# Kernel optimization log

Hardware: AMD Instinct MI355X
Metric: run time of the kernel (lower is better)

## Reference

```python
import jax, jax.numpy as jnp
import numpy as np

B, S, D, C = 16, 1024, 768, 2


def setup_inputs() -> dict:
    key = jax.random.key(0)
    ks = jax.random.split(key, 6)
    sc = 1.0 / np.sqrt(D)
    return {
        "tokens": jax.random.normal(ks[0], (B, S, D), jnp.float32),
        "Wk": jax.random.normal(ks[1], (D, D), jnp.float32) * sc,
        "bk": jnp.zeros((D,), jnp.float32),
        "Wq": jax.random.normal(ks[2], (D, D), jnp.float32) * sc,
        "bq": jnp.zeros((D,), jnp.float32),
        "Wv": jax.random.normal(ks[3], (D, D), jnp.float32) * sc,
        "bv": jnp.zeros((D,), jnp.float32),
        "ln_g": jnp.ones((S, D), jnp.float32),
        "ln_b": jnp.zeros((S, D), jnp.float32),
        "W_sgsa": jax.random.normal(ks[4], (D, 1), jnp.float32) * sc,
        "b_sgsa": jnp.zeros((1,), jnp.float32),
        "W_fnn": jax.random.normal(ks[5], (4 * D, C), jnp.float32) * (1.0 / np.sqrt(4 * D)),
        "b_fnn": jnp.zeros((C,), jnp.float32),
    }


def reference(tokens, Wk, bk, Wq, bq, Wv, bv, ln_g, ln_b, W_sgsa, b_sgsa, W_fnn, b_fnn):
    fact = 1.0 / jnp.sqrt(jnp.asarray(D, tokens.dtype))
    # --- token-wise single-head attention ---
    K = tokens @ Wk + bk                                  # [B,S,D]
    Q = tokens @ Wq + bq
    V = tokens @ Wv + bv
    att = jax.nn.softmax(jnp.einsum('bsd,btd->bst', Q, K) * fact, axis=-1)  # [B,S,S]
    out = jnp.einsum('bst,btd->bsd', att, V)              # [B,S,D]
    # --- LayerNorm over last two dims (S,D) jointly, eps=1e-8 ---
    mu = jnp.mean(out, axis=(1, 2), keepdims=True)
    var = jnp.var(out, axis=(1, 2), keepdims=True)
    out_ln = (out - mu) / jnp.sqrt(var + 1e-8) * ln_g + ln_b
    # --- feature-wise attention (same K/Q/V weights, transposed bmm) ---
    K_N = out_ln @ Wk + bk
    Q_N = out_ln @ Wq + bq
    V_N = out_ln @ Wv + bv
    att_N = jax.nn.softmax(jnp.einsum('bsd,bse->bde', Q_N, K_N) * fact, axis=-1)  # [B,D,D]
    out_N = jnp.einsum('bsd,bde->bse', V_N, att_N)        # [B,S,D]
    # --- SGSA gating ---
    gate = out_N @ W_sgsa + b_sgsa                        # [B,S,1]
    out_sgsa = gate * out_N                               # [B,S,D]
    # --- concat, dual pooling, FC ---
    cat = jnp.concatenate([tokens, out_sgsa], axis=2)     # [B,S,2D]
    pooled = jnp.concatenate([jnp.mean(cat, axis=1), jnp.max(cat, axis=1)], axis=1)  # [B,4D]
    return pooled @ W_fnn + b_fnn                         # [B,C]
```

## Files before the change

### kernel.cpp

```cpp
#include <hip/hip_runtime.h>

#define BB 16
#define SS 1024
#define DD 768

typedef _Float16 f16x4 __attribute__((ext_vector_type(4)));
typedef _Float16 f16x8 __attribute__((ext_vector_type(8)));
typedef float f32x4 __attribute__((ext_vector_type(4)));

__device__ __forceinline__ void gload_lds16(const void* g, void* l) {
  __builtin_amdgcn_global_load_lds(
      (const __attribute__((address_space(1))) unsigned int*)g,
      (__attribute__((address_space(3))) unsigned int*)l, 16, 0, 0);
}

template<int OUTM, int BIAS>
__global__ __launch_bounds__(512) void gemm256(
    const _Float16* __restrict__ A, long long aB,
    const _Float16* __restrict__ Bt, long long bB,
    const float* __restrict__ bias, int biasB,
    void* __restrict__ Cv, long long cB,
    int M, int N, int K)
{
  __shared__ __attribute__((aligned(16))) _Float16 lds[65536];
  const int t = threadIdx.x;
  int z, m0, n0;
  if (OUTM == 3 || OUTM == 4) {
    z = blockIdx.x / 3;
    n0 = (blockIdx.x % 3) * 256;
    m0 = blockIdx.y * 256;
  } else {
    z = blockIdx.z;
    m0 = blockIdx.x * 256;
    n0 = blockIdx.y * 256;
  }
  const _Float16* Ab = A + (size_t)z * aB;
  const _Float16* Bb = Bt + (size_t)z * bB;

  const int l = t & 63, w = t >> 6;
  const int wr = (w >> 2) * 128, wc = (w & 3) * 64;
  const int lrow = l & 15, kq = l >> 4;
  const int p2 = lrow >> 1;
  const int qread = ((lrow & 1) << 2) | (kq ^ (p2 & 3));
  const int fragoff = p2 * 128 + qread * 16;

  const int sp = t >> 3, sq = t & 7;
  const int srow = 2 * sp + (sq >> 2);
  const int schk = (sq & 3) ^ (sp & 3);
  const size_t ldK = (size_t)K * 2;
  const char* pA0 = (const char*)Ab + (size_t)(m0 + srow) * ldK + schk * 16;
  const char* pA1 = pA0 + (size_t)128 * ldK;
  const char* pB0 = (const char*)Bb + (size_t)(n0 + srow) * ldK + schk * 16;
  const char* pB1 = pB0 + (size_t)128 * ldK;
  char* const ldsb = (char*)lds;
  const int dstt = t * 16;

  auto stg = [&](int mat, int s, int T, int sd) {
    const char* g0 = (mat ? pB0 : pA0) + (size_t)T * 128 + s * 64;
    const char* g1 = (mat ? pB1 : pA1) + (size_t)T * 128 + s * 64;
    char* d = ldsb + sd * 65536 + mat * 32768 + s * 16384 + dstt;
    gload_lds16(g0, d);
    gload_lds16(g1, d + 8192);
  };

  f32x4 acc[8][4] = {};
  f16x8 af[4], bfr[4];

#define LOAD_B(S) { _Pragma("unroll") for (int n = 0; n < 4; n++) \
    bfr[n] = *(const f16x8*)(Bbase + (S) * 16384 + (wc + n * 16) * 64 + fragoff); }
#define LOAD_A(S, QM) { _Pragma("unroll") for (int mi = 0; mi < 4; mi++) \
    af[mi] = *(const f16x8*)(Abase + (S) * 16384 + (wr + (QM) * 64 + mi * 16) * 64 + fragoff); }
#define MFMA16(QM) { __builtin_amdgcn_s_setprio(1); \
    _Pragma("unroll") for (int mi = 0; mi < 4; mi++) { \
      _Pragma("unroll") for (int n = 0; n < 4; n++) \
        acc[(QM) * 4 + mi][n] = __builtin_amdgcn_mfma_f32_16x16x32_f16( \
            af[mi], bfr[n], acc[(QM) * 4 + mi][n], 0, 0, 0); } \
    __builtin_amdgcn_s_setprio(0); }

  stg(0, 0, 0, 0); stg(1, 0, 0, 0); stg(0, 1, 0, 0); stg(1, 1, 0, 0);

  const int NT = K >> 6;
  for (int T = 0; T < NT; ++T) {
    const int sd = T & 1, sn = sd ^ 1;
    const char* Abase = ldsb + sd * 65536;
    const char* Bbase = Abase + 32768;
    const bool pf = (T + 1) < NT;

    asm volatile("s_waitcnt vmcnt(4)" ::: "memory");
    __builtin_amdgcn_s_barrier();
    asm volatile("" ::: "memory");
    if (pf) stg(0, 0, T + 1, sn);
    LOAD_B(0)
    LOAD_A(0, 0)
    MFMA16(0)
    __builtin_amdgcn_s_barrier();
    asm volatile("" ::: "memory");
    if (pf) stg(1, 0, T + 1, sn);
    LOAD_A(0, 1)
    MFMA16(1)
    if (pf) asm volatile("s_waitcnt vmcnt(4)" ::: "memory");
    else    asm volatile("s_waitcnt vmcnt(0)" ::: "memory");
    __builtin_amdgcn_s_barrier();
    asm volatile("" ::: "memory");
    if (pf) stg(0, 1, T + 1, sn);
    LOAD_B(1)
    LOAD_A(1, 0)
    MFMA16(0)
    __builtin_amdgcn_s_barrier();
    asm volatile("" ::: "memory");
    if (pf) stg(1, 1, T + 1, sn);
    LOAD_A(1, 1)
    MFMA16(1)
  }
#undef LOAD_A
#undef LOAD_B
#undef MFMA16

  const int crow = (l >> 4) * 4, ccol = l & 15;
  #pragma unroll
  for (int m = 0; m < 8; ++m) {
    const int rq = m0 + wr + (m >> 2) * 64 + (m & 3) * 16 + crow;
    #pragma unroll
    for (int n = 0; n < 4; ++n) {
      const int c = n0 + wc + n * 16 + ccol;
      const float bv = BIAS ? bias[(size_t)z * biasB + c] : 0.0f;
      if (OUTM == 0) {
        float* C = (float*)Cv + (size_t)z * cB;
        #pragma unroll
        for (int j = 0; j < 4; j++)
          C[(size_t)(rq + j) * N + c] = acc[m][n][j] + bv;
      } else {
        _Float16* C = (_Float16*)Cv + (size_t)z * cB;
        const bool tr = (OUTM == 3) ? (z == 2) : (z < 2);
        if (tr) {
          const int bq = rq >> 10, s = rq & 1023;
          f16x4 o;
          #pragma unroll
          for (int j = 0; j < 4; j++) o[j] = (_Float16)(acc[m][n][j] + bv);
          *(f16x4*)&C[((size_t)(bq * N + c) << 10) + s] = o;
        } else {
          #pragma unroll
          for (int j = 0; j < 4; j++)
            C[(size_t)(rq + j) * N + c] = (_Float16)(acc[m][n][j] + bv);
        }
      }
    }
  }
}

__global__ __launch_bounds__(256) void cast_f2h(const float* __restrict__ in,
                                                _Float16* __restrict__ outp, long long n4)
{
  for (long long i = (long long)blockIdx.x * 256 + threadIdx.x; i < n4;
       i += (long long)gridDim.x * 256) {
    float4 v = ((const float4*)in)[i];
    f16x4 r;
    r[0] = (_Float16)v.x; r[1] = (_Float16)v.y; r[2] = (_Float16)v.z; r[3] = (_Float16)v.w;
    ((f16x4*)outp)[i] = r;
  }
}

__global__ __launch_bounds__(256) void transpose_f2h(const float* __restrict__ in,
                                                     _Float16* __restrict__ outp, int R, int C)
{
  __shared__ float tile[32][33];
  const int r0 = blockIdx.y * 32, c0 = blockIdx.x * 32;
  const int tx = threadIdx.x & 31, ty = threadIdx.x >> 5;
  #pragma unroll
  for (int i = 0; i < 4; i++)
    tile[ty + i * 8][tx] = in[(size_t)(r0 + ty + i * 8) * C + c0 + tx];
  __syncthreads();
  #pragma unroll
  for (int i = 0; i < 4; i++)
    outp[(size_t)(c0 + ty + i * 8) * R + r0 + tx] = (_Float16)tile[tx][ty + i * 8];
}

__global__ __launch_bounds__(256) void transpose_b2h(const _Float16* __restrict__ in, long long inB,
                                                     _Float16* __restrict__ outp, long long outB,
                                                     int R, int C)
{
  __shared__ _Float16 tile[32][33];
  const _Float16* ib = in + (size_t)blockIdx.z * inB;
  _Float16* ob = outp + (size_t)blockIdx.z * outB;
  const int r0 = blockIdx.y * 32, c0 = blockIdx.x * 32;
  const int tx = threadIdx.x & 31, ty = threadIdx.x >> 5;
  #pragma unroll
  for (int i = 0; i < 4; i++)
    tile[ty + i * 8][tx] = ib[(size_t)(r0 + ty + i * 8) * C + c0 + tx];
  __syncthreads();
  #pragma unroll
  for (int i = 0; i < 4; i++)
    ob[(size_t)(c0 + ty + i * 8) * R + r0 + tx] = tile[tx][ty + i * 8];
}

__global__ void pack_bias(const float* __restrict__ a, const float* __restrict__ b,
                          const float* __restrict__ c, float* __restrict__ o)
{
  int t = blockIdx.x * 256 + threadIdx.x;
  if (t < 768) o[t] = a[t];
  else if (t < 1536) o[t] = b[t - 768];
  else if (t < 2304) o[t] = c[t - 1536];
}

template<int VPT>
__global__ __launch_bounds__(256) void softmax_f2h(const float* __restrict__ X,
                                                   _Float16* __restrict__ Y,
                                                   int L, float scale)
{
  const size_t base = (size_t)blockIdx.x * L;
  const int t = threadIdx.x;
  float v[VPT];
  float m = -3.4e38f;
  #pragma unroll
  for (int j = 0; j < VPT; j++) { v[j] = X[base + t + j * 256]; m = fmaxf(m, v[j]); }
  __shared__ float red[256];
  red[t] = m; __syncthreads();
  #pragma unroll
  for (int off = 128; off > 0; off >>= 1) {
    if (t < off) red[t] = fmaxf(red[t], red[t + off]);
    __syncthreads();
  }
  m = red[0]; __syncthreads();
  float s = 0.0f;
  #pragma unroll
  for (int j = 0; j < VPT; j++) { v[j] = __expf((v[j] - m) * scale); s += v[j]; }
  red[t] = s; __syncthreads();
  #pragma unroll
  for (int off = 128; off > 0; off >>= 1) {
    if (t < off) red[t] += red[t + off];
    __syncthreads();
  }
  const float inv = 1.0f / red[0];
  #pragma unroll
  for (int j = 0; j < VPT; j++) Y[base + t + j * 256] = (_Float16)(v[j] * inv);
}

__global__ __launch_bounds__(256) void ln_partial(const float* __restrict__ src,
                                                  float* __restrict__ part)
{
  const int b = blockIdx.y, ch = blockIdx.x;
  const float4* p = (const float4*)(src + (size_t)b * SS * DD) + (size_t)ch * 3072;
  const int t = threadIdx.x;
  float s = 0.0f, q = 0.0f;
  #pragma unroll
  for (int i = 0; i < 12; i++) {
    float4 v = p[t + i * 256];
    s += v.x + v.y + v.z + v.w;
    q += v.x * v.x + v.y * v.y + v.z * v.z + v.w * v.w;
  }
  __shared__ float rs[256], rq[256];
  rs[t] = s; rq[t] = q; __syncthreads();
  #pragma unroll
  for (int off = 128; off > 0; off >>= 1) {
    if (t < off) { rs[t] += rs[t + off]; rq[t] += rq[t + off]; }
    __syncthreads();
  }
  if (t == 0) { part[(b * 64 + ch) * 2] = rs[0]; part[(b * 64 + ch) * 2 + 1] = rq[0]; }
}

__global__ void ln_final(const float* __restrict__ part, float* __restrict__ stats)
{
  const int b = blockIdx.x, t = threadIdx.x;
  float s = part[(b * 64 + t) * 2];
  float q = part[(b * 64 + t) * 2 + 1];
  #pragma unroll
  for (int off = 32; off > 0; off >>= 1) { s += __shfl_down(s, off); q += __shfl_down(q, off); }
  if (t == 0) {
    const float invN = 1.0f / (float)(SS * DD);
    float mu = s * invN;
    float var = q * invN - mu * mu;
    stats[b * 2] = mu;
    stats[b * 2 + 1] = rsqrtf(var + 1e-8f);
  }
}

__global__ __launch_bounds__(256) void ln_apply_h(const float* __restrict__ src,
                                                  const float* __restrict__ g,
                                                  const float* __restrict__ bta,
                                                  const float* __restrict__ stats,
                                                  _Float16* __restrict__ dst)
{
  const long long n4 = (long long)BB * SS * DD / 4;
  const int SD4 = SS * DD / 4;
  for (long long i = (long long)blockIdx.x * 256 + threadIdx.x; i < n4;
       i += (long long)gridDim.x * 256) {
    const int b = (int)(i / SD4);
    const int sd4 = (int)(i - (long long)b * SD4);
    const float mu = stats[b * 2], rs = stats[b * 2 + 1];
    float4 v = ((const float4*)src)[i];
    float4 gg = ((const float4*)g)[sd4];
    float4 bb = ((const float4*)bta)[sd4];
    f16x4 r;
    r[0] = (_Float16)((v.x - mu) * rs * gg.x + bb.x);
    r[1] = (_Float16)((v.y - mu) * rs * gg.y + bb.y);
    r[2] = (_Float16)((v.z - mu) * rs * gg.z + bb.z);
    r[3] = (_Float16)((v.w - mu) * rs * gg.w + bb.w);
    ((f16x4*)dst)[i] = r;
  }
}

__global__ __launch_bounds__(256) void gate_k(const float* __restrict__ outN,
                                              const float* __restrict__ wsg,
                                              const float* __restrict__ bsg,
                                              float* __restrict__ gate)
{
  const int row = blockIdx.x * 4 + (threadIdx.x >> 6);
  const int l = threadIdx.x & 63;
  const float* src = outN + (size_t)row * DD;
  float s = 0.0f;
  #pragma unroll
  for (int i = 0; i < 12; i++) s += src[l + i * 64] * wsg[l + i * 64];
  #pragma unroll
  for (int off = 32; off > 0; off >>= 1) s += __shfl_down(s, off);
  if (l == 0) gate[row] = s + bsg[0];
}

__global__ __launch_bounds__(256) void pool_partial(const float* __restrict__ tokens,
                                                    const float* __restrict__ outN,
                                                    const float* __restrict__ gate,
                                                    float* __restrict__ part)
{
  const int b = blockIdx.y, ch = blockIdx.x, t = threadIdx.x;
  float st0 = 0, st1 = 0, st2 = 0, so0 = 0, so1 = 0, so2 = 0;
  float xt0 = -3.4e38f, xt1 = -3.4e38f, xt2 = -3.4e38f;
  float xo0 = -3.4e38f, xo1 = -3.4e38f, xo2 = -3.4e38f;
  const size_t rowbase = ((size_t)b * SS + ch * 32) * DD;
  for (int i = 0; i < 32; i++) {
    const float* tr = tokens + rowbase + (size_t)i * DD;
    const float* orw = outN + rowbase + (size_t)i * DD;
    const float g = gate[b * SS + ch * 32 + i];
    float t0 = tr[t], t1 = tr[t + 256], t2 = tr[t + 512];
    float o0 = orw[t] * g, o1 = orw[t + 256] * g, o2 = orw[t + 512] * g;
    st0 += t0; st1 += t1; st2 += t2;
    so0 += o0; so1 += o1; so2 += o2;
    xt0 = fmaxf(xt0, t0); xt1 = fmaxf(xt1, t1); xt2 = fmaxf(xt2, t2);
    xo0 = fmaxf(xo0, o0); xo1 = fmaxf(xo1, o1); xo2 = fmaxf(xo2, o2);
  }
  float* pb = part + (size_t)(b * 32 + ch) * 3072;
  pb[t] = st0;          pb[t + 256] = st1;          pb[t + 512] = st2;
  pb[768 + t] = so0;    pb[768 + t + 256] = so1;    pb[768 + t + 512] = so2;
  pb[1536 + t] = xt0;   pb[1536 + t + 256] = xt1;   pb[1536 + t + 512] = xt2;
  pb[2304 + t] = xo0;   pb[2304 + t + 256] = xo1;   pb[2304 + t + 512] = xo2;
}

__global__ __launch_bounds__(256) void pool_final(const float* __restrict__ part,
                                                  float* __restrict__ pooled)
{
  const int idx = blockIdx.x * 256 + threadIdx.x;
  const int b = idx / DD, d = idx - b * DD;
  float st = 0, so = 0, xt = -3.4e38f, xo = -3.4e38f;
  for (int ch = 0; ch < 32; ch++) {
    const float* pb = part + (size_t)(b * 32 + ch) * 3072;
    st += pb[d]; so += pb[768 + d];
    xt = fmaxf(xt, pb[1536 + d]); xo = fmaxf(xo, pb[2304 + d]);
  }
  const float inv = 1.0f / (float)SS;
  pooled[(size_t)b * 3072 + d]        = st * inv;
  pooled[(size_t)b * 3072 + 768 + d]  = so * inv;
  pooled[(size_t)b * 3072 + 1536 + d] = xt;
  pooled[(size_t)b * 3072 + 2304 + d] = xo;
}

__global__ __launch_bounds__(256) void fc_k(const float* __restrict__ pooled,
                                            const float* __restrict__ Wf,
                                            const float* __restrict__ bf,
                                            float* __restrict__ outp)
{
  const int b = blockIdx.x, t = threadIdx.x;
  float p0 = 0.0f, p1 = 0.0f;
  #pragma unroll
  for (int i = 0; i < 12; i++) {
    const int j = t + i * 256;
    const float pv = pooled[(size_t)b * 3072 + j];
    p0 += pv * Wf[j * 2];
    p1 += pv * Wf[j * 2 + 1];
  }
  __shared__ float r0[256], r1[256];
  r0[t] = p0; r1[t] = p1; __syncthreads();
  #pragma unroll
  for (int off = 128; off > 0; off >>= 1) {
    if (t < off) { r0[t] += r0[t + off]; r1[t] += r1[t + off]; }
    __syncthreads();
  }
  if (t == 0) {
    outp[b * 2 + 0] = r0[0] + bf[0];
    outp[b * 2 + 1] = r1[0] + bf[1];
  }
}

extern "C" void kernel_launch(void* const* d_in, const int* in_sizes, int n_in,
                              void* d_out, int out_size, void* d_ws, size_t ws_size,
                              hipStream_t stream)
{
  const float* tokens = (const float*)d_in[0];
  const float* Wk  = (const float*)d_in[1];
  const float* bk  = (const float*)d_in[2];
  const float* Wq  = (const float*)d_in[3];
  const float* bq  = (const float*)d_in[4];
  const float* Wv  = (const float*)d_in[5];
  const float* bv  = (const float*)d_in[6];
  const float* lng = (const float*)d_in[7];
  const float* lnb = (const float*)d_in[8];
  const float* Wsg = (const float*)d_in[9];
  const float* bsg = (const float*)d_in[10];
  const float* Wf  = (const float*)d_in[11];
  const float* bfn = (const float*)d_in[12];
  float* outp = (float*)d_out;
  (void)in_sizes; (void)n_in; (void)out_size; (void)ws_size;

  char* ws = (char*)d_ws;
  float*    R0   = (float*)(ws + 0);
  _Float16* R1   = (_Float16*)(ws + 67108864);
  _Float16* R2   = (_Float16*)(ws + 92274688);
  _Float16* R3   = (_Float16*)(ws + 117440512);
  _Float16* R4   = (_Float16*)(ws + 142606336);
  _Float16* R5   = (_Float16*)(ws + 167772160);
  _Float16* Wt   = (_Float16*)(ws + 201326592);
  float* bias3   = (float*)(ws + 204865536);
  float* part    = (float*)(ws + 204874752);
  float* stats   = (float*)(ws + 204882944);
  float* gate    = (float*)(ws + 204883072);
  float* ppart   = (float*)(ws + 204948608);
  float* pooled  = (float*)(ws + 211240064);

  const float fact = 0.036084391824351615f;
  const long long SD = (long long)SS * DD;
  const long long S2 = (long long)SS * SS;
  const long long D2 = (long long)DD * DD;
  const long long PL = (long long)BB * SD;

  cast_f2h<<<2048, 256, 0, stream>>>(tokens, R1, PL / 4);
  transpose_f2h<<<dim3(24, 24), 256, 0, stream>>>(Wk, Wt,               768, 768);
  transpose_f2h<<<dim3(24, 24), 256, 0, stream>>>(Wq, Wt + 589824,      768, 768);
  transpose_f2h<<<dim3(24, 24), 256, 0, stream>>>(Wv, Wt + 2 * 589824,  768, 768);
  pack_bias<<<9, 256, 0, stream>>>(bk, bq, bv, bias3);

  gemm256<3, 1><<<dim3(9, 64, 1), 512, 0, stream>>>(R1, 0, Wt, 589824, bias3, 768,
                                                    (void*)R2, PL, BB * SS, DD, DD);
  gemm256<0, 0><<<dim3(4, 4, 16), 512, 0, stream>>>(R3, SD, R2, SD, nullptr, 0,
                                                    (void*)R0, S2, SS, SS, DD);
  softmax_f2h<4><<<BB * SS, 256, 0, stream>>>(R0, R5, SS, fact);
  gemm256<0, 0><<<dim3(4, 3, 16), 512, 0, stream>>>(R5, S2, R4, SD, nullptr, 0,
                                                    (void*)R0, SD, SS, DD, SS);
  ln_partial<<<dim3(64, 16), 256, 0, stream>>>(R0, part);
  ln_final<<<16, 64, 0, stream>>>(part, stats);
  ln_apply_h<<<2048, 256, 0, stream>>>(R0, lng, lnb, stats, R1);

  gemm256<4, 1><<<dim3(9, 64, 1), 512, 0, stream>>>(R1, 0, Wt, 589824, bias3, 768,
                                                    (void*)R2, PL, BB * SS, DD, DD);
  gemm256<0, 0><<<dim3(3, 3, 16), 512, 0, stream>>>(R3, SD, R2, SD, nullptr, 0,
                                                    (void*)R0, D2, DD, DD, SS);
  softmax_f2h<3><<<BB * DD, 256, 0, stream>>>(R0, R5, DD, fact);
  transpose_b2h<<<dim3(24, 24, 16), 256, 0, stream>>>(R5, D2, R1, D2, DD, DD);
  gemm256<0, 0><<<dim3(4, 3, 16), 512, 0, stream>>>(R4, SD, R1, D2, nullptr, 0,
                                                    (void*)R0, SD, SS, DD, DD);

  gate_k<<<4096, 256, 0, stream>>>(R0, Wsg, bsg, gate);
  pool_partial<<<dim3(32, BB), 256, 0, stream>>>(tokens, R0, gate, ppart);
  pool_final<<<48, 256, 0, stream>>>(ppart, pooled);
  fc_k<<<16, 256, 0, stream>>>(pooled, Wf, bfn, outp);
}
```

Measured before the change: 451.8 us.

## Merge GEMM half-phases to halve barriers and remap blocks per XCD

The 256x256 GEMM main loop now loads both A sub-fragments at once and issues 32 MFMAs per phase. This removes two of the four block barriers per K-tile, and both A and B stage copies are issued together. For the projection GEMMs (OUTM 3/4) the block index is remapped so that consecutive M tiles sharing the same z/n tiles land on the same XCD, to improve L2 reuse. The trade-offs are 16 extra VGPRs for the second A fragment set and coarser overlap between LDS staging and compute.

```diff
diff --git a/kernel.cpp b/kernel.cpp
--- a/kernel.cpp
+++ b/kernel.cpp
@@ -26,9 +26,13 @@
   const int t = threadIdx.x;
   int z, m0, n0;
   if (OUTM == 3 || OUTM == 4) {
-    z = blockIdx.x / 3;
-    n0 = (blockIdx.x % 3) * 256;
-    m0 = blockIdx.y * 256;
+    const int lin = blockIdx.x + 9 * blockIdx.y;
+    const int xcd = lin & 7, idx = lin >> 3;
+    const int mt  = xcd * 8 + idx / 9;
+    const int zn  = idx % 9;
+    z  = zn / 3;
+    n0 = (zn % 3) * 256;
+    m0 = mt * 256;
   } else {
     z = blockIdx.z;
     m0 = blockIdx.x * 256;
@@ -64,17 +68,23 @@
   };
 
   f32x4 acc[8][4] = {};
-  f16x8 af[4], bfr[4];
+  f16x8 a0f[4], a1f[4], bfr[4];
 
 #define LOAD_B(S) { _Pragma("unroll") for (int n = 0; n < 4; n++) \
     bfr[n] = *(const f16x8*)(Bbase + (S) * 16384 + (wc + n * 16) * 64 + fragoff); }
-#define LOAD_A(S, QM) { _Pragma("unroll") for (int mi = 0; mi < 4; mi++) \
-    af[mi] = *(const f16x8*)(Abase + (S) * 16384 + (wr + (QM) * 64 + mi * 16) * 64 + fragoff); }
-#define MFMA16(QM) { __builtin_amdgcn_s_setprio(1); \
+#define LOAD_A0(S) { _Pragma("unroll") for (int mi = 0; mi < 4; mi++) \
+    a0f[mi] = *(const f16x8*)(Abase + (S) * 16384 + (wr + mi * 16) * 64 + fragoff); }
+#define LOAD_A1(S) { _Pragma("unroll") for (int mi = 0; mi < 4; mi++) \
+    a1f[mi] = *(const f16x8*)(Abase + (S) * 16384 + (wr + 64 + mi * 16) * 64 + fragoff); }
+#define MFMA32 { __builtin_amdgcn_s_setprio(1); \
     _Pragma("unroll") for (int mi = 0; mi < 4; mi++) { \
       _Pragma("unroll") for (int n = 0; n < 4; n++) \
-        acc[(QM) * 4 + mi][n] = __builtin_amdgcn_mfma_f32_16x16x32_f16( \
-            af[mi], bfr[n], acc[(QM) * 4 + mi][n], 0, 0, 0); } \
+        acc[mi][n] = __builtin_amdgcn_mfma_f32_16x16x32_f16( \
+            a0f[mi], bfr[n], acc[mi][n], 0, 0, 0); } \
+    _Pragma("unroll") for (int mi = 0; mi < 4; mi++) { \
+      _Pragma("unroll") for (int n = 0; n < 4; n++) \
+        acc[4 + mi][n] = __builtin_amdgcn_mfma_f32_16x16x32_f16( \
+            a1f[mi], bfr[n], acc[4 + mi][n], 0, 0, 0); } \
     __builtin_amdgcn_s_setprio(0); }
 
   stg(0, 0, 0, 0); stg(1, 0, 0, 0); stg(0, 1, 0, 0); stg(1, 1, 0, 0);
@@ -89,32 +99,25 @@
     asm volatile("s_waitcnt vmcnt(4)" ::: "memory");
     __builtin_amdgcn_s_barrier();
     asm volatile("" ::: "memory");
-    if (pf) stg(0, 0, T + 1, sn);
+    if (pf) { stg(0, 0, T + 1, sn); stg(1, 0, T + 1, sn); }
     LOAD_B(0)
-    LOAD_A(0, 0)
-    MFMA16(0)
-    __builtin_amdgcn_s_barrier();
-    asm volatile("" ::: "memory");
-    if (pf) stg(1, 0, T + 1, sn);
-    LOAD_A(0, 1)
-    MFMA16(1)
+    LOAD_A0(0)
+    LOAD_A1(0)
+    MFMA32
     if (pf) asm volatile("s_waitcnt vmcnt(4)" ::: "memory");
     else    asm volatile("s_waitcnt vmcnt(0)" ::: "memory");
     __builtin_amdgcn_s_barrier();
     asm volatile("" ::: "memory");
-    if (pf) stg(0, 1, T + 1, sn);
+    if (pf) { stg(0, 1, T + 1, sn); stg(1, 1, T + 1, sn); }
     LOAD_B(1)
-    LOAD_A(1, 0)
-    MFMA16(0)
-    __builtin_amdgcn_s_barrier();
-    asm volatile("" ::: "memory");
-    if (pf) stg(1, 1, T + 1, sn);
-    LOAD_A(1, 1)
-    MFMA16(1)
-  }
-#undef LOAD_A
+    LOAD_A0(1)
+    LOAD_A1(1)
+    MFMA32
+  }
 #undef LOAD_B
-#undef MFMA16
+#undef LOAD_A0
+#undef LOAD_A1
+#undef MFMA32
 
   const int crow = (l >> 4) * 4, ccol = l & 15;
   #pragma unroll
```

New measurement: 441.1 us. 2.4% less time.
